# Kernel optimization log

Hardware: AMD Instinct MI355X
Metric: run time of the kernel (lower is better)

## Reference

```python
import jax, jax.numpy as jnp
import numpy as np

C = 64          # channels
K = 15          # sum(shell_sizes)=1+14
H = 32          # neighbors per query
N = 50000       # support points (== query points M)
RADIUS = 1.0
SIGMA = 0.7
INF = 1e6
BN_EPS = 1e-5


def _init_kernel_points(key):
    # stand-in for load_kernels: 1 center point + 14 points on a sphere shell
    pts = jax.random.normal(key, (K - 1, 3), dtype=jnp.float32)
    pts = pts / jnp.linalg.norm(pts, axis=1, keepdims=True) * RADIUS
    return jnp.concatenate([jnp.zeros((1, 3), jnp.float32), pts], axis=0)


def setup_inputs() -> dict:
    key = jax.random.key(0)
    ks = jax.random.split(key, 10)
    q_pts = jax.random.normal(ks[0], (N, 3), dtype=jnp.float32)
    s_pts = jax.random.normal(ks[1], (N, 3), dtype=jnp.float32)
    s_feats = jax.random.normal(ks[2], (N, C), dtype=jnp.float32)
    neighb_inds = jax.random.randint(ks[3], (N, H), 0, N)
    kernel_points = _init_kernel_points(ks[4])
    # alpha_mlp: Linear(C->C, no bias) -> BatchNorm -> LeakyReLU(0.1) -> Linear(C->K*C)
    lim1 = 1.0 / np.sqrt(C)
    W1 = jax.random.uniform(ks[5], (C, C), jnp.float32, -lim1, lim1)
    gamma = jnp.ones((C,), jnp.float32)
    beta = jnp.zeros((C,), jnp.float32)
    W2 = jax.random.uniform(ks[6], (C, K * C), jnp.float32, -lim1, lim1)
    b2 = jax.random.uniform(ks[7], (K * C,), jnp.float32, -lim1, lim1)
    return {"q_pts": q_pts, "s_pts": s_pts, "s_feats": s_feats,
            "neighb_inds": neighb_inds, "kernel_points": kernel_points,
            "W1": W1, "gamma": gamma, "beta": beta, "W2": W2, "b2": b2}


def reference(q_pts, s_pts, s_feats, neighb_inds, kernel_points, W1, gamma, beta, W2, b2):
    M = q_pts.shape[0]
    # alpha_mlp on pooled (= center) features: (M, C) -> (M, K*C)
    h = s_feats @ W1
    mu = jnp.mean(h, axis=0)
    var = jnp.var(h, axis=0)
    h = (h - mu) / jnp.sqrt(var + BN_EPS) * gamma + beta
    h = jax.nn.leaky_relu(h, 0.1)
    conv_weights = (h @ W2 + b2).reshape(M, K, C)

    # gather neighbor features with a zero padding row (index N -> zeros)
    padded_feats = jnp.concatenate([s_feats, jnp.zeros((1, C), s_feats.dtype)], axis=0)
    neighbor_feats = padded_feats[neighb_inds]                 # (M, H, C)

    # relative neighbor positions with inf padding point
    s_pts_pad = jnp.concatenate([s_pts, jnp.full((1, 3), INF, s_pts.dtype)], axis=0)
    neighbors = s_pts_pad[neighb_inds] - q_pts[:, None, :]     # (M, H, 3)

    # kernel-point influence: nearest kernel point + linear influence
    diff = neighbors[:, :, None, :] - kernel_points            # (M, H, K, 3)
    sq_d = jnp.sum(diff * diff, axis=-1)                       # (M, H, K)
    nn_sq = jnp.min(sq_d, axis=-1)                             # (M, H)
    nn_idx = jnp.argmin(sq_d, axis=-1)                         # (M, H)
    infl = jnp.clip(1.0 - jnp.sqrt(nn_sq) / SIGMA, 0.0)        # (M, H)

    # per-neighbor channel weights from the MLP output, gathered by 1nn kernel point
    nw = jnp.take_along_axis(conv_weights, nn_idx[:, :, None], axis=1)  # (M, H, C)
    nw = nw * infl[:, :, None]

    # weighted aggregation (merge=mul, aggr=sum over neighbors)
    return jnp.sum(neighbor_feats * nw, axis=1)                # (M, C)
```

## Files before the change

### kernel.cpp

```cpp
#include <hip/hip_runtime.h>
#include <math.h>

#define N_PTS 50000
#define CCH   64
#define KP    15
#define NH    32
#define SIGMA 0.7f
#define BN_EPS 1e-5f
#define LEAKY 0.1f
#define QB    16
#define CWS   17
#define STATS_BLOCKS 1024

typedef short bf16x8 __attribute__((ext_vector_type(8)));
typedef float floatx4 __attribute__((ext_vector_type(4)));

__device__ __forceinline__ unsigned short f2b(float f) {
    union { float f; unsigned u; } v; v.f = f;
    return (unsigned short)((v.u + 0x7FFFu + ((v.u >> 16) & 1u)) >> 16);
}
__device__ __forceinline__ float b2f(unsigned short b) {
    union { unsigned u; float f; } v; v.u = ((unsigned)b) << 16;
    return v.f;
}

__global__ __launch_bounds__(256) void k_prep(const float* __restrict__ sf,
                                              const float* __restrict__ W1,
                                              const float* __restrict__ W2,
                                              float* __restrict__ bn,
                                              unsigned short* __restrict__ hst,
                                              unsigned short* __restrict__ w2b) {
    int t = threadIdx.x;
    if (blockIdx.x >= STATS_BLOCKS) {
        int g = (blockIdx.x - STATS_BLOCKS) * 256 + t;
        int lane = g & 63, s = (g >> 6) & 1, tt = g >> 7;
        int col = lane & 15, quad = lane >> 4;
        int base = (s * 32 + quad * 8) * 960 + tt * 16 + col;
        ushort4 lo, hi;
        lo.x = f2b(W2[base + 0 * 960]); lo.y = f2b(W2[base + 1 * 960]);
        lo.z = f2b(W2[base + 2 * 960]); lo.w = f2b(W2[base + 3 * 960]);
        hi.x = f2b(W2[base + 4 * 960]); hi.y = f2b(W2[base + 5 * 960]);
        hi.z = f2b(W2[base + 6 * 960]); hi.w = f2b(W2[base + 7 * 960]);
        *(ushort4*)(w2b + g * 8)     = lo;
        *(ushort4*)(w2b + g * 8 + 4) = hi;
        return;
    }
    int c = t & 63, ml = t >> 6;
    float w1c[64];
    #pragma unroll
    for (int i = 0; i < 64; ++i) w1c[i] = W1[i * 64 + c];
    __shared__ float rows[4][64];
    float acc_s = 0.f, acc_q = 0.f;
    for (int m0 = blockIdx.x * 4; m0 < N_PTS; m0 += STATS_BLOCKS * 4) {
        __syncthreads();
        ((float*)rows)[t] = sf[m0 * 64 + t];
        __syncthreads();
        float h = 0.f;
        #pragma unroll
        for (int i4 = 0; i4 < 16; ++i4) {
            float4 r = *(const float4*)&rows[ml][i4 * 4];
            h += r.x * w1c[i4 * 4] + r.y * w1c[i4 * 4 + 1]
               + r.z * w1c[i4 * 4 + 2] + r.w * w1c[i4 * 4 + 3];
        }
        acc_s += h;
        acc_q += h * h;
        hst[(m0 + ml) * 64 + c] = f2b(h);
    }
    __shared__ float red[2][256];
    red[0][t] = acc_s; red[1][t] = acc_q;
    __syncthreads();
    if (t < 64) {
        float s = red[0][t] + red[0][64 + t] + red[0][128 + t] + red[0][192 + t];
        float q = red[1][t] + red[1][64 + t] + red[1][128 + t] + red[1][192 + t];
        atomicAdd(&bn[t], s);
        atomicAdd(&bn[64 + t], q);
    }
}

__global__ __launch_bounds__(512, 4) void k_main(
    const float* __restrict__ q_pts, const float* __restrict__ s_pts,
    const float* __restrict__ s_feats, const int* __restrict__ nb,
    const float* __restrict__ kpts, const float* __restrict__ gamma,
    const float* __restrict__ beta, const float* __restrict__ bn,
    const float* __restrict__ b2, const unsigned short* __restrict__ w2b,
    const unsigned short* __restrict__ hst, float* __restrict__ out) {

    __shared__ __align__(16) unsigned short cwT[960 * CWS];
    __shared__ float abS[128];
    __shared__ float kp[48];
    __shared__ int      nCnt[QB];
    __shared__ unsigned nPack[QB][NH];

    int t = threadIdx.x;
    int lane = t & 63, wv = t >> 6;
    int m0 = blockIdx.x * QB;

    if (t < 64) {
        float mu  = bn[t] * (1.0f / N_PTS);
        float var = bn[64 + t] * (1.0f / N_PTS) - mu * mu;
        float a   = gamma[t] * rsqrtf(var + BN_EPS);
        abS[t]      = a;
        abS[64 + t] = beta[t] - mu * a;
    } else if (t >= 64 && t < 64 + 45) {
        kp[t - 64] = kpts[t - 64];
    } else if (t >= 128 && t < 128 + QB) {
        nCnt[t - 128] = 0;
    }
    ((unsigned*)nPack)[t] = 0u;
    __syncthreads();

    int q1 = t >> 5, hh = t & 31;
    int m1 = m0 + q1;
    int idx = nb[m1 * NH + hh];
    float qx = q_pts[m1 * 3 + 0], qy = q_pts[m1 * 3 + 1], qz = q_pts[m1 * 3 + 2];

    int row = lane & 15, half = lane >> 4;
    const unsigned short* hrow = hst + (m0 + row) * 64 + half * 8;
    bf16x8 r0 = *(const bf16x8*)(hrow);
    bf16x8 r1 = *(const bf16x8*)(hrow + 32);

    bf16x8 a0, a1;
    #pragma unroll
    for (int j = 0; j < 8; ++j) {
        int c0 = half * 8 + j;
        float g0 = abS[c0] * b2f((unsigned short)r0[j]) + abS[64 + c0];
        g0 = g0 > 0.f ? g0 : LEAKY * g0;
        a0[j] = (short)f2b(g0);
        int c1 = 32 + c0;
        float g1 = abS[c1] * b2f((unsigned short)r1[j]) + abS[64 + c1];
        g1 = g1 > 0.f ? g1 : LEAKY * g1;
        a1[j] = (short)f2b(g1);
    }

    float sx = s_pts[idx * 3 + 0];
    float sy = s_pts[idx * 3 + 1];
    float sz = s_pts[idx * 3 + 2];

    {
        int col = lane & 15, quad = lane >> 4;
        for (int tt = wv; tt < 60; tt += 8) {
            bf16x8 bf0 = *(const bf16x8*)(w2b + ((tt * 2 + 0) * 64 + lane) * 8);
            bf16x8 bf1 = *(const bf16x8*)(w2b + ((tt * 2 + 1) * 64 + lane) * 8);
            floatx4 acc = {0.f, 0.f, 0.f, 0.f};
            acc = __builtin_amdgcn_mfma_f32_16x16x32_bf16(a0, bf0, acc, 0, 0, 0);
            acc = __builtin_amdgcn_mfma_f32_16x16x32_bf16(a1, bf1, acc, 0, 0, 0);
            int n = tt * 16 + col;
            float bb = b2[n];
            unsigned short* dst = &cwT[n * CWS + quad * 4];
            ushort2 w01, w23;
            w01.x = f2b(acc[0] + bb); w01.y = f2b(acc[1] + bb);
            w23.x = f2b(acc[2] + bb); w23.y = f2b(acc[3] + bb);
            *(ushort2*)(dst)     = w01;
            *(ushort2*)(dst + 2) = w23;
        }
    }

    {
        float px = sx - qx, py = sy - qy, pz = sz - qz;
        float best = 1e30f; int bi = 0;
        #pragma unroll
        for (int k = 0; k < KP; ++k) {
            float dx = px - kp[k * 3], dy = py - kp[k * 3 + 1], dz = pz - kp[k * 3 + 2];
            float d = dx * dx + dy * dy + dz * dz;
            if (d < best) { best = d; bi = k; }
        }
        float infl = 1.f - sqrtf(best) * (1.0f / SIGMA);
        if (infl > 0.f) {
            int iq = (int)(infl * 4095.f + 0.5f);
            int pos = atomicAdd(&nCnt[q1], 1);
            nPack[q1][pos] = (unsigned)idx | ((unsigned)bi << 16) | ((unsigned)iq << 20);
        }
    }
    __syncthreads();

    {
        int qa = wv * 2, qb = wv * 2 + 1;
        int c = lane;
        int naA = nCnt[qa], naB = nCnt[qb];
        int na = naA > naB ? naA : naB;
        float accA = 0.f, accB = 0.f;
        for (int jj = 0; jj < na; jj += 2) {
            uint2 pa = *(const uint2*)&nPack[qa][jj];
            uint2 pb = *(const uint2*)&nPack[qb][jj];
            float fA0 = s_feats[(pa.x & 0xFFFFu) * 64 + c];
            float fA1 = s_feats[(pa.y & 0xFFFFu) * 64 + c];
            float fB0 = s_feats[(pb.x & 0xFFFFu) * 64 + c];
            float fB1 = s_feats[(pb.y & 0xFFFFu) * 64 + c];
            float wA0 = b2f(cwT[(((pa.x >> 16) & 15u) * 64 + c) * CWS + qa]);
            float wA1 = b2f(cwT[(((pa.y >> 16) & 15u) * 64 + c) * CWS + qa]);
            float wB0 = b2f(cwT[(((pb.x >> 16) & 15u) * 64 + c) * CWS + qb]);
            float wB1 = b2f(cwT[(((pb.y >> 16) & 15u) * 64 + c) * CWS + qb]);
            float iA0 = (float)(pa.x >> 20) * (1.f / 4095.f);
            float iA1 = (float)(pa.y >> 20) * (1.f / 4095.f);
            float iB0 = (float)(pb.x >> 20) * (1.f / 4095.f);
            float iB1 = (float)(pb.y >> 20) * (1.f / 4095.f);
            accA += iA0 * fA0 * wA0 + iA1 * fA1 * wA1;
            accB += iB0 * fB0 * wB0 + iB1 * fB1 * wB1;
        }
        out[(m0 + qa) * 64 + c] = accA;
        out[(m0 + qb) * 64 + c] = accB;
    }
}

extern "C" void kernel_launch(void* const* d_in, const int* in_sizes, int n_in,
                              void* d_out, int out_size, void* d_ws, size_t ws_size,
                              hipStream_t stream) {
    const float* q_pts   = (const float*)d_in[0];
    const float* s_pts   = (const float*)d_in[1];
    const float* s_feats = (const float*)d_in[2];
    const int*   nb      = (const int*)d_in[3];
    const float* kpts    = (const float*)d_in[4];
    const float* W1      = (const float*)d_in[5];
    const float* gamma   = (const float*)d_in[6];
    const float* beta    = (const float*)d_in[7];
    const float* W2      = (const float*)d_in[8];
    const float* b2      = (const float*)d_in[9];
    float* out = (float*)d_out;

    float* ws = (float*)d_ws;
    float* bn = ws;
    unsigned short* w2b = (unsigned short*)(ws + 128);
    unsigned short* hst = w2b + 61440;

    hipMemsetAsync(bn, 0, 128 * sizeof(float), stream);
    k_prep<<<STATS_BLOCKS + 30, 256, 0, stream>>>(s_feats, W1, W2, bn, hst, w2b);
    k_main<<<N_PTS / QB, 512, 0, stream>>>(q_pts, s_pts, s_feats, nb, kpts,
                                           gamma, beta, bn, b2, w2b, hst, out);
}
```

Measured before the change: 186.0 us.

## Halve k_main block size to 256 threads, doubling per-thread work

k_main now runs with 256 threads (4 waves) per 16-query block instead of 512. Each thread handles two neighbor slots in the kernel-point search, each wave computes 15 MFMA tiles of the conv-weight matrix, and each wave aggregates four queries per channel lane. The influence dequantization scale is hoisted out of the inner loop and applied once at the end. The intent is lower per-block overhead and more independent gathers in flight per thread, at the cost of more registers and less thread-level parallelism per block.

```diff
diff --git a/kernel.cpp b/kernel.cpp
--- a/kernel.cpp
+++ b/kernel.cpp
@@ -77,7 +77,7 @@
     }
 }
 
-__global__ __launch_bounds__(512, 4) void k_main(
+__global__ __launch_bounds__(256, 4) void k_main(
     const float* __restrict__ q_pts, const float* __restrict__ s_pts,
     const float* __restrict__ s_feats, const int* __restrict__ nb,
     const float* __restrict__ kpts, const float* __restrict__ gamma,
@@ -101,18 +101,21 @@
         float a   = gamma[t] * rsqrtf(var + BN_EPS);
         abS[t]      = a;
         abS[64 + t] = beta[t] - mu * a;
-    } else if (t >= 64 && t < 64 + 45) {
+    } else if (t < 64 + 45) {
         kp[t - 64] = kpts[t - 64];
-    } else if (t >= 128 && t < 128 + QB) {
-        nCnt[t - 128] = 0;
-    }
-    ((unsigned*)nPack)[t] = 0u;
+    } else if (t >= 112 && t < 112 + QB) {
+        nCnt[t - 112] = 0;
+    }
+    ((unsigned*)nPack)[t]       = 0u;
+    ((unsigned*)nPack)[t + 256] = 0u;
     __syncthreads();
 
-    int q1 = t >> 5, hh = t & 31;
-    int m1 = m0 + q1;
-    int idx = nb[m1 * NH + hh];
-    float qx = q_pts[m1 * 3 + 0], qy = q_pts[m1 * 3 + 1], qz = q_pts[m1 * 3 + 2];
+    int qA = t >> 5,        hA = t & 31;        int mA = m0 + qA;
+    int qBq = (t + 256) >> 5, hB = t & 31;      int mB = m0 + qBq;
+    int idxA = nb[mA * NH + hA];
+    int idxB = nb[mB * NH + hB];
+    float qAx = q_pts[mA * 3 + 0], qAy = q_pts[mA * 3 + 1], qAz = q_pts[mA * 3 + 2];
+    float qBx = q_pts[mB * 3 + 0], qBy = q_pts[mB * 3 + 1], qBz = q_pts[mB * 3 + 2];
 
     int row = lane & 15, half = lane >> 4;
     const unsigned short* hrow = hst + (m0 + row) * 64 + half * 8;
@@ -132,13 +135,13 @@
         a1[j] = (short)f2b(g1);
     }
 
-    float sx = s_pts[idx * 3 + 0];
-    float sy = s_pts[idx * 3 + 1];
-    float sz = s_pts[idx * 3 + 2];
+    float sAx = s_pts[idxA * 3 + 0], sAy = s_pts[idxA * 3 + 1], sAz = s_pts[idxA * 3 + 2];
+    float sBx = s_pts[idxB * 3 + 0], sBy = s_pts[idxB * 3 + 1], sBz = s_pts[idxB * 3 + 2];
 
     {
         int col = lane & 15, quad = lane >> 4;
-        for (int tt = wv; tt < 60; tt += 8) {
+        for (int ti = 0; ti < 15; ++ti) {
+            int tt = wv * 15 + ti;
             bf16x8 bf0 = *(const bf16x8*)(w2b + ((tt * 2 + 0) * 64 + lane) * 8);
             bf16x8 bf1 = *(const bf16x8*)(w2b + ((tt * 2 + 1) * 64 + lane) * 8);
             floatx4 acc = {0.f, 0.f, 0.f, 0.f};
@@ -156,7 +159,7 @@
     }
 
     {
-        float px = sx - qx, py = sy - qy, pz = sz - qz;
+        float px = sAx - qAx, py = sAy - qAy, pz = sAz - qAz;
         float best = 1e30f; int bi = 0;
         #pragma unroll
         for (int k = 0; k < KP; ++k) {
@@ -167,38 +170,68 @@
         float infl = 1.f - sqrtf(best) * (1.0f / SIGMA);
         if (infl > 0.f) {
             int iq = (int)(infl * 4095.f + 0.5f);
-            int pos = atomicAdd(&nCnt[q1], 1);
-            nPack[q1][pos] = (unsigned)idx | ((unsigned)bi << 16) | ((unsigned)iq << 20);
+            int pos = atomicAdd(&nCnt[qA], 1);
+            nPack[qA][pos] = (unsigned)idxA | ((unsigned)bi << 16) | ((unsigned)iq << 20);
+        }
+        px = sBx - qBx; py = sBy - qBy; pz = sBz - qBz;
+        best = 1e30f; bi = 0;
+        #pragma unroll
+        for (int k = 0; k < KP; ++k) {
+            float dx = px - kp[k * 3], dy = py - kp[k * 3 + 1], dz = pz - kp[k * 3 + 2];
+            float d = dx * dx + dy * dy + dz * dz;
+            if (d < best) { best = d; bi = k; }
+        }
+        infl = 1.f - sqrtf(best) * (1.0f / SIGMA);
+        if (infl > 0.f) {
+            int iq = (int)(infl * 4095.f + 0.5f);
+            int pos = atomicAdd(&nCnt[qBq], 1);
+            nPack[qBq][pos] = (unsigned)idxB | ((unsigned)bi << 16) | ((unsigned)iq << 20);
         }
     }
     __syncthreads();
 
     {
-        int qa = wv * 2, qb = wv * 2 + 1;
+        int q0 = wv * 4, q1 = q0 + 1, q2 = q0 + 2, q3 = q0 + 3;
         int c = lane;
-        int naA = nCnt[qa], naB = nCnt[qb];
-        int na = naA > naB ? naA : naB;
-        float accA = 0.f, accB = 0.f;
+        int n01 = nCnt[q0] > nCnt[q1] ? nCnt[q0] : nCnt[q1];
+        int n23 = nCnt[q2] > nCnt[q3] ? nCnt[q2] : nCnt[q3];
+        int na  = n01 > n23 ? n01 : n23;
+        float acc0 = 0.f, acc1 = 0.f, acc2 = 0.f, acc3 = 0.f;
         for (int jj = 0; jj < na; jj += 2) {
-            uint2 pa = *(const uint2*)&nPack[qa][jj];
-            uint2 pb = *(const uint2*)&nPack[qb][jj];
-            float fA0 = s_feats[(pa.x & 0xFFFFu) * 64 + c];
-            float fA1 = s_feats[(pa.y & 0xFFFFu) * 64 + c];
-            float fB0 = s_feats[(pb.x & 0xFFFFu) * 64 + c];
-            float fB1 = s_feats[(pb.y & 0xFFFFu) * 64 + c];
-            float wA0 = b2f(cwT[(((pa.x >> 16) & 15u) * 64 + c) * CWS + qa]);
-            float wA1 = b2f(cwT[(((pa.y >> 16) & 15u) * 64 + c) * CWS + qa]);
-            float wB0 = b2f(cwT[(((pb.x >> 16) & 15u) * 64 + c) * CWS + qb]);
-            float wB1 = b2f(cwT[(((pb.y >> 16) & 15u) * 64 + c) * CWS + qb]);
-            float iA0 = (float)(pa.x >> 20) * (1.f / 4095.f);
-            float iA1 = (float)(pa.y >> 20) * (1.f / 4095.f);
-            float iB0 = (float)(pb.x >> 20) * (1.f / 4095.f);
-            float iB1 = (float)(pb.y >> 20) * (1.f / 4095.f);
-            accA += iA0 * fA0 * wA0 + iA1 * fA1 * wA1;
-            accB += iB0 * fB0 * wB0 + iB1 * fB1 * wB1;
-        }
-        out[(m0 + qa) * 64 + c] = accA;
-        out[(m0 + qb) * 64 + c] = accB;
+            uint2 p0 = *(const uint2*)&nPack[q0][jj];
+            uint2 p1 = *(const uint2*)&nPack[q1][jj];
+            uint2 p2 = *(const uint2*)&nPack[q2][jj];
+            uint2 p3 = *(const uint2*)&nPack[q3][jj];
+            float f00 = s_feats[(p0.x & 0xFFFFu) * 64 + c];
+            float f01 = s_feats[(p0.y & 0xFFFFu) * 64 + c];
+            float f10 = s_feats[(p1.x & 0xFFFFu) * 64 + c];
+            float f11 = s_feats[(p1.y & 0xFFFFu) * 64 + c];
+            float f20 = s_feats[(p2.x & 0xFFFFu) * 64 + c];
+            float f21 = s_feats[(p2.y & 0xFFFFu) * 64 + c];
+            float f30 = s_feats[(p3.x & 0xFFFFu) * 64 + c];
+            float f31 = s_feats[(p3.y & 0xFFFFu) * 64 + c];
+            float w00 = b2f(cwT[(((p0.x >> 16) & 15u) * 64 + c) * CWS + q0]);
+            float w01 = b2f(cwT[(((p0.y >> 16) & 15u) * 64 + c) * CWS + q0]);
+            float w10 = b2f(cwT[(((p1.x >> 16) & 15u) * 64 + c) * CWS + q1]);
+            float w11 = b2f(cwT[(((p1.y >> 16) & 15u) * 64 + c) * CWS + q1]);
+            float w20 = b2f(cwT[(((p2.x >> 16) & 15u) * 64 + c) * CWS + q2]);
+            float w21 = b2f(cwT[(((p2.y >> 16) & 15u) * 64 + c) * CWS + q2]);
+            float w30 = b2f(cwT[(((p3.x >> 16) & 15u) * 64 + c) * CWS + q3]);
+            float w31 = b2f(cwT[(((p3.y >> 16) & 15u) * 64 + c) * CWS + q3]);
+            float i00 = (float)(p0.x >> 20), i01 = (float)(p0.y >> 20);
+            float i10 = (float)(p1.x >> 20), i11 = (float)(p1.y >> 20);
+            float i20 = (float)(p2.x >> 20), i21 = (float)(p2.y >> 20);
+            float i30 = (float)(p3.x >> 20), i31 = (float)(p3.y >> 20);
+            acc0 += i00 * f00 * w00 + i01 * f01 * w01;
+            acc1 += i10 * f10 * w10 + i11 * f11 * w11;
+            acc2 += i20 * f20 * w20 + i21 * f21 * w21;
+            acc3 += i30 * f30 * w30 + i31 * f31 * w31;
+        }
+        const float qs = 1.f / 4095.f;
+        out[(m0 + q0) * 64 + c] = acc0 * qs;
+        out[(m0 + q1) * 64 + c] = acc1 * qs;
+        out[(m0 + q2) * 64 + c] = acc2 * qs;
+        out[(m0 + q3) * 64 + c] = acc3 * qs;
     }
 }
 
@@ -224,6 +257,6 @@
 
     hipMemsetAsync(bn, 0, 128 * sizeof(float), stream);
     k_prep<<<STATS_BLOCKS + 30, 256, 0, stream>>>(s_feats, W1, W2, bn, hst, w2b);
-    k_main<<<N_PTS / QB, 512, 0, stream>>>(q_pts, s_pts, s_feats, nb, kpts,
+    k_main<<<N_PTS / QB, 256, 0, stream>>>(q_pts, s_pts, s_feats, nb, kpts,
                                            gamma, beta, bn, b2, w2b, hst, out);
 }
```

After: 189.2 us. Within noise of the previous version (+1.7%).
